# Kernel optimization log

Hardware: AMD Instinct MI355X
Metric: run time of the kernel (lower is better)

Reference implementation:

```python
import jax, jax.numpy as jnp
from jax import lax
import numpy as np

PADDING = 1
STRIDE = 1


def setup_inputs() -> dict:
    key = jax.random.key(0)
    k1, k2 = jax.random.split(key)
    x = jax.random.normal(k1, (256, 224, 224), dtype=jnp.float32)       # [C, H, W]
    kernel = jax.random.normal(k2, (256, 256, 3, 3), dtype=jnp.float32)  # [O, C, kh, kw]
    return {"x": x, "kernel": kernel}


def reference(x, kernel):
    # Direct conv2d with zero padding and stride, equivalent to the
    # nested-loop torch implementation (cross-correlation, no bias).
    out = lax.conv_general_dilated(
        x[None],                      # [1, C, H, W]
        kernel,                       # [O, C, kh, kw]
        window_strides=(STRIDE, STRIDE),
        padding=[(PADDING, PADDING), (PADDING, PADDING)],
        dimension_numbers=("NCHW", "OIHW", "NCHW"),
    )
    return out[0]                     # [O, Hout, Wout]
```

## Files before the change

kernel.cpp:

```cpp
#include <hip/hip_runtime.h>
#include <hip/hip_bf16.h>
#include <stdint.h>

#define C_IN  256
#define C_OUT 256
#define H_IN  224
#define W_IN  224
#define HP    226
#define WP    226
#define NPIX  (H_IN * W_IN)
#define BM    128
#define BN    128
#define BK    64

typedef __attribute__((ext_vector_type(8))) short short8;
typedef __attribute__((ext_vector_type(4))) float f32x4;

__device__ __forceinline__ unsigned short f2bf(float f) {
    __hip_bfloat16 b = __float2bfloat16(f);
    return *(unsigned short*)&b;
}

__device__ __forceinline__ void gl_lds16(const unsigned short* g, unsigned short* l) {
    __builtin_amdgcn_global_load_lds(
        (const __attribute__((address_space(1))) unsigned int*)g,
        (__attribute__((address_space(3))) unsigned int*)l,
        16, 0, 0);
}


__global__ void zero_border(unsigned short* __restrict__ xp) {
    int i = blockIdx.x * 256 + threadIdx.x;
    uint4 z = make_uint4(0u, 0u, 0u, 0u);
    if (i < 7232) {
        ((uint4*)xp)[i] = z;
    } else if (i < 14464) {
        ((uint4*)(xp + (size_t)225 * WP * C_IN))[i - 7232] = z;
    } else if (i < 21632) {
        int j = i - 14464; int h = 1 + (j >> 5); int c4 = j & 31;
        ((uint4*)(xp + ((size_t)h * WP) * C_IN))[c4] = z;
    } else if (i < 28800) {
        int j = i - 21632; int h = 1 + (j >> 5); int c4 = j & 31;
        ((uint4*)(xp + ((size_t)h * WP + 225) * C_IN))[c4] = z;
    }
}

__global__ void prep_x(const float* __restrict__ x, unsigned short* __restrict__ xp) {
    int b  = blockIdx.x;
    int ct = b & 3, wt = (b >> 2) & 3, h = b >> 4;
    int c0 = ct * 64, w0 = wt * 64;
    int t  = threadIdx.x;
    __shared__ float tile[64][65];

    int w   = t & 63;
    int cl0 = t >> 6;
    #pragma unroll
    for (int i = 0; i < 16; ++i) {
        int cl = i * 4 + cl0;
        float v = 0.f;
        if (w0 + w < W_IN)
            v = x[(size_t)(c0 + cl) * NPIX + (size_t)h * W_IN + w0 + w];
        tile[cl][w] = v;
    }
    __syncthreads();

    int wc = t >> 2;
    int cc = (t & 3) * 16;
    if (w0 + wc < W_IN) {
        uint32_t pk[8];
        #pragma unroll
        for (int j = 0; j < 8; ++j) {
            unsigned short lo = f2bf(tile[cc + 2 * j][wc]);
            unsigned short hi = f2bf(tile[cc + 2 * j + 1][wc]);
            pk[j] = (uint32_t)lo | ((uint32_t)hi << 16);
        }
        size_t base = ((size_t)(h + 1) * WP + (w0 + wc + 1)) * C_IN + c0 + cc;
        uint4* dst = (uint4*)(xp + base);
        dst[0] = make_uint4(pk[0], pk[1], pk[2], pk[3]);
        dst[1] = make_uint4(pk[4], pk[5], pk[6], pk[7]);
    }
}

__global__ void prep_w(const float* __restrict__ wk, unsigned short* __restrict__ wb) {
    int idx = blockIdx.x * 256 + threadIdx.x;
    int c = idx & 255, o = (idx >> 8) & 255, p = idx >> 16;
    wb[((size_t)p * 256 + o) * 256 + c] = f2bf(wk[((size_t)o * 256 + c) * 9 + p]);
}


__launch_bounds__(256, 2)
__global__ void conv_gemm(const unsigned short* __restrict__ xp,
                          const unsigned short* __restrict__ wb,
                          float* __restrict__ out) {
    int wgid = (blockIdx.x & 7) * 98 + (blockIdx.x >> 3);
    int mt = wgid & 1;
    int nt = wgid >> 1;
    int m0 = mt * BM;
    int n0 = nt * BN;
    int t  = threadIdx.x;
    int l  = t & 63, wv = t >> 6;

    __shared__ __align__(16) unsigned short lds[2 * 16384];

    int q8 = ((l & 7) ^ (l >> 3)) * 8;
    int rA = l >> 3;
    int offA0, offA1, offA2, offA3, offB0, offB1, offB2, offB3;
    {
        int r0 = (wv * 4 + 0) * 8 + rA;
        int r1 = (wv * 4 + 1) * 8 + rA;
        int r2 = (wv * 4 + 2) * 8 + rA;
        int r3 = (wv * 4 + 3) * 8 + rA;
        offA0 = (m0 + r0) * C_IN + q8;
        offA1 = (m0 + r1) * C_IN + q8;
        offA2 = (m0 + r2) * C_IN + q8;
        offA3 = (m0 + r3) * C_IN + q8;
        int nc0 = n0 + r0, nc1 = n0 + r1, nc2 = n0 + r2, nc3 = n0 + r3;
        int h0 = nc0 / W_IN, h1 = nc1 / W_IN, h2 = nc2 / W_IN, h3 = nc3 / W_IN;
        offB0 = (h0 * WP + (nc0 - h0 * W_IN)) * C_IN + q8;
        offB1 = (h1 * WP + (nc1 - h1 * W_IN)) * C_IN + q8;
        offB2 = (h2 * WP + (nc2 - h2 * W_IN)) * C_IN + q8;
        offB3 = (h3 * WP + (nc3 - h3 * W_IN)) * C_IN + q8;
    }

    int la = l & 15;
    int lk = l >> 4;
    int mo = (wv >> 1) * 64;
    int no = (wv & 1) * 64;
    int xq0 = ((0 * 4 + lk) ^ (la & 7)) * 8;
    int xq1 = ((1 * 4 + lk) ^ (la & 7)) * 8;

    f32x4 acc[4][4];
    #pragma unroll
    for (int i = 0; i < 4; ++i)
        #pragma unroll
        for (int j = 0; j < 4; ++j)
            acc[i][j] = f32x4{0.f, 0.f, 0.f, 0.f};

#define STAGE(BD, S) do {                                                    \
    int s_ = (S);                                                            \
    int p_ = s_ >> 2, cs_ = (s_ & 3) << 6;                                   \
    int kh_ = (p_ * 11) >> 5; int kw_ = p_ - 3 * kh_;                        \
    const unsigned short* aS_ = wb + p_ * 65536 + cs_;                       \
    const unsigned short* bS_ = xp + (kh_ * WP + kw_) * C_IN + cs_;          \
    gl_lds16(aS_ + offA0, &lds[(BD) * 16384 + (wv * 4 + 0) * 512]);          \
    gl_lds16(aS_ + offA1, &lds[(BD) * 16384 + (wv * 4 + 1) * 512]);          \
    gl_lds16(aS_ + offA2, &lds[(BD) * 16384 + (wv * 4 + 2) * 512]);          \
    gl_lds16(aS_ + offA3, &lds[(BD) * 16384 + (wv * 4 + 3) * 512]);          \
    gl_lds16(bS_ + offB0, &lds[(BD) * 16384 + 8192 + (wv * 4 + 0) * 512]);   \
    gl_lds16(bS_ + offB1, &lds[(BD) * 16384 + 8192 + (wv * 4 + 1) * 512]);   \
    gl_lds16(bS_ + offB2, &lds[(BD) * 16384 + 8192 + (wv * 4 + 2) * 512]);   \
    gl_lds16(bS_ + offB3, &lds[(BD) * 16384 + 8192 + (wv * 4 + 3) * 512]);   \
} while (0)

#define COMPUTE(BC) do {                                                     \
    short8 af_[4][2], bf_[4][2];                                             \
    _Pragma("unroll")                                                        \
    for (int i_ = 0; i_ < 4; ++i_) {                                         \
        af_[i_][0] = *(const short8*)&lds[(BC) * 16384 + (mo + i_ * 16 + la) * BK + xq0]; \
        af_[i_][1] = *(const short8*)&lds[(BC) * 16384 + (mo + i_ * 16 + la) * BK + xq1]; \
    }                                                                        \
    _Pragma("unroll")                                                        \
    for (int i_ = 0; i_ < 4; ++i_) {                                         \
        bf_[i_][0] = *(const short8*)&lds[(BC) * 16384 + 8192 + (no + i_ * 16 + la) * BK + xq0]; \
        bf_[i_][1] = *(const short8*)&lds[(BC) * 16384 + 8192 + (no + i_ * 16 + la) * BK + xq1]; \
    }                                                                        \
    __builtin_amdgcn_s_setprio(1);                                           \
    _Pragma("unroll")                                                        \
    for (int i_ = 0; i_ < 4; ++i_)                                           \
        _Pragma("unroll")                                                    \
        for (int j_ = 0; j_ < 4; ++j_)                                       \
            acc[i_][j_] = __builtin_amdgcn_mfma_f32_16x16x32_bf16(           \
                af_[i_][0], bf_[j_][0], acc[i_][j_], 0, 0, 0);               \
    _Pragma("unroll")                                                        \
    for (int i_ = 0; i_ < 4; ++i_)                                           \
        _Pragma("unroll")                                                    \
        for (int j_ = 0; j_ < 4; ++j_)                                       \
            acc[i_][j_] = __builtin_amdgcn_mfma_f32_16x16x32_bf16(           \
                af_[i_][1], bf_[j_][1], acc[i_][j_], 0, 0, 0);               \
    __builtin_amdgcn_s_setprio(0);                                           \
} while (0)

#define GUARD_IN(VMSTR) do {                                                 \
    asm volatile("s_waitcnt " VMSTR ::: "memory");                           \
    __builtin_amdgcn_sched_barrier(0);                                       \
    __builtin_amdgcn_s_barrier();                                            \
    __builtin_amdgcn_sched_barrier(0);                                       \
} while (0)

#define GUARD_OUT() do {                                                     \
    asm volatile("s_waitcnt lgkmcnt(0)" ::: "memory");                       \
    __builtin_amdgcn_sched_barrier(0);                                       \
    __builtin_amdgcn_s_barrier();                                            \
    __builtin_amdgcn_sched_barrier(0);                                       \
} while (0)

#define BODY(BC, S) do {                                                     \
    STAGE((BC) ^ 1, (S) + 1);                                                \
    GUARD_IN("vmcnt(8)");                                                    \
    COMPUTE(BC);                                                             \
    GUARD_OUT();                                                             \
} while (0)

    STAGE(0, 0);
    #pragma unroll 1
    for (int k = 0; k < 17; ++k) {
        BODY(0, 2 * k);
        BODY(1, 2 * k + 1);
    }
    BODY(0, 34);
    GUARD_IN("vmcnt(0)");
    COMPUTE(1);

#undef BODY
#undef GUARD_OUT
#undef GUARD_IN
#undef COMPUTE
#undef STAGE

    int ro = lk * 4;
    #pragma unroll
    for (int i = 0; i < 4; ++i) {
        #pragma unroll
        for (int j = 0; j < 4; ++j) {
            int oo = m0 + mo + i * 16 + ro;
            int nn = n0 + no + j * 16 + la;
            #pragma unroll
            for (int r = 0; r < 4; ++r)
                out[(size_t)(oo + r) * NPIX + nn] = acc[i][j][r];
        }
    }
}

__global__ void conv_naive(const float* __restrict__ x, const float* __restrict__ wk,
                           float* __restrict__ out) {
    int idx = blockIdx.x * 256 + threadIdx.x;
    int n = idx % NPIX;
    int o = idx / NPIX;
    int h = n / W_IN, w = n - (n / W_IN) * W_IN;
    float s = 0.f;
    for (int c = 0; c < C_IN; ++c) {
        const float* xc = x + (size_t)c * NPIX;
        const float* wc = wk + ((size_t)o * C_IN + c) * 9;
        #pragma unroll
        for (int kh = 0; kh < 3; ++kh) {
            int hh = h + kh - 1;
            if (hh < 0 || hh >= H_IN) continue;
            #pragma unroll
            for (int kw = 0; kw < 3; ++kw) {
                int ww = w + kw - 1;
                if (ww < 0 || ww >= W_IN) continue;
                s += xc[hh * W_IN + ww] * wc[kh * 3 + kw];
            }
        }
    }
    out[idx] = s;
}

extern "C" void kernel_launch(void* const* d_in, const int* in_sizes, int n_in,
                              void* d_out, int out_size, void* d_ws, size_t ws_size,
                              hipStream_t stream) {
    const float* x  = (const float*)d_in[0];
    const float* wk = (const float*)d_in[1];
    float* out = (float*)d_out;

    const size_t xp_elems = (size_t)HP * WP * C_IN;
    const size_t wb_elems = (size_t)9 * 256 * 256;
    const size_t need = (xp_elems + wb_elems) * 2;

    if (ws_size < need) {
        conv_naive<<<(C_OUT * NPIX) / 256, 256, 0, stream>>>(x, wk, out);
        return;
    }

    unsigned short* xp = (unsigned short*)d_ws;
    unsigned short* wb = xp + xp_elems;

    zero_border<<<113, 256, 0, stream>>>(xp);
    prep_x<<<224 * 16, 256, 0, stream>>>(x, xp);
    prep_w<<<2304, 256, 0, stream>>>(wk, wb);
    conv_gemm<<<392 * 2, 256, 0, stream>>>(xp, wb, out);
}
```

Measured before the change: 88.47 us.

## Merge weight prep with border zeroing and split LDS reads around MFMA halves

Weight conversion and border zeroing now run as one launch instead of two, removing one kernel launch. The GEMM main loop is reorganised: each iteration waits for the previous prefetch, loads half of the K fragments from LDS, issues the next stage's global-to-LDS prefetch, runs 16 MFMAs, then loads the second half and runs the rest. This interleaves LDS reads with MFMA work and trims register pressure. The trade-off is vmcnt(0) at the top of every iteration, so the prefetch now has only one compute phase to hide behind instead of overlapping freely.

```diff
diff --git a/kernel.cpp b/kernel.cpp
--- a/kernel.cpp
+++ b/kernel.cpp
@@ -29,8 +29,16 @@
 }
 
 
-__global__ void zero_border(unsigned short* __restrict__ xp) {
-    int i = blockIdx.x * 256 + threadIdx.x;
+__global__ void prep_misc(const float* __restrict__ wk, unsigned short* __restrict__ wb,
+                          unsigned short* __restrict__ xp) {
+    int b = blockIdx.x;
+    if (b < 2304) {
+        int idx = b * 256 + threadIdx.x;
+        int c = idx & 255, o = (idx >> 8) & 255, p = idx >> 16;
+        wb[((size_t)p * 256 + o) * 256 + c] = f2bf(wk[((size_t)o * 256 + c) * 9 + p]);
+        return;
+    }
+    int i = (b - 2304) * 256 + threadIdx.x;
     uint4 z = make_uint4(0u, 0u, 0u, 0u);
     if (i < 7232) {
         ((uint4*)xp)[i] = z;
@@ -79,12 +87,6 @@
         dst[0] = make_uint4(pk[0], pk[1], pk[2], pk[3]);
         dst[1] = make_uint4(pk[4], pk[5], pk[6], pk[7]);
     }
-}
-
-__global__ void prep_w(const float* __restrict__ wk, unsigned short* __restrict__ wb) {
-    int idx = blockIdx.x * 256 + threadIdx.x;
-    int c = idx & 255, o = (idx >> 8) & 255, p = idx >> 16;
-    wb[((size_t)p * 256 + o) * 256 + c] = f2bf(wk[((size_t)o * 256 + c) * 9 + p]);
 }
 
 
@@ -152,69 +154,60 @@
     gl_lds16(bS_ + offB3, &lds[(BD) * 16384 + 8192 + (wv * 4 + 3) * 512]);   \
 } while (0)
 
-#define COMPUTE(BC) do {                                                     \
-    short8 af_[4][2], bf_[4][2];                                             \
-    _Pragma("unroll")                                                        \
-    for (int i_ = 0; i_ < 4; ++i_) {                                         \
-        af_[i_][0] = *(const short8*)&lds[(BC) * 16384 + (mo + i_ * 16 + la) * BK + xq0]; \
-        af_[i_][1] = *(const short8*)&lds[(BC) * 16384 + (mo + i_ * 16 + la) * BK + xq1]; \
-    }                                                                        \
-    _Pragma("unroll")                                                        \
-    for (int i_ = 0; i_ < 4; ++i_) {                                         \
-        bf_[i_][0] = *(const short8*)&lds[(BC) * 16384 + 8192 + (no + i_ * 16 + la) * BK + xq0]; \
-        bf_[i_][1] = *(const short8*)&lds[(BC) * 16384 + 8192 + (no + i_ * 16 + la) * BK + xq1]; \
-    }                                                                        \
+#define MFMA16(AF, BF) do {                                                  \
     __builtin_amdgcn_s_setprio(1);                                           \
     _Pragma("unroll")                                                        \
     for (int i_ = 0; i_ < 4; ++i_)                                           \
         _Pragma("unroll")                                                    \
         for (int j_ = 0; j_ < 4; ++j_)                                       \
             acc[i_][j_] = __builtin_amdgcn_mfma_f32_16x16x32_bf16(           \
-                af_[i_][0], bf_[j_][0], acc[i_][j_], 0, 0, 0);               \
+                AF[i_], BF[j_], acc[i_][j_], 0, 0, 0);                       \
+    __builtin_amdgcn_s_setprio(0);                                           \
+} while (0)
+
+#define LGKM0() do {                                                         \
+    asm volatile("s_waitcnt lgkmcnt(0)" ::: "memory");                       \
+    __builtin_amdgcn_sched_barrier(0);                                       \
+} while (0)
+
+#define BODY(BC, S, DO_STAGE) do {                                           \
+    asm volatile("s_waitcnt vmcnt(0)" ::: "memory");                         \
+    __builtin_amdgcn_sched_barrier(0);                                       \
+    __builtin_amdgcn_s_barrier();                                            \
+    __builtin_amdgcn_sched_barrier(0);                                       \
+    short8 a0_[4], b0_[4], a1_[4], b1_[4];                                   \
     _Pragma("unroll")                                                        \
-    for (int i_ = 0; i_ < 4; ++i_)                                           \
-        _Pragma("unroll")                                                    \
-        for (int j_ = 0; j_ < 4; ++j_)                                       \
-            acc[i_][j_] = __builtin_amdgcn_mfma_f32_16x16x32_bf16(           \
-                af_[i_][1], bf_[j_][1], acc[i_][j_], 0, 0, 0);               \
-    __builtin_amdgcn_s_setprio(0);                                           \
-} while (0)
-
-#define GUARD_IN(VMSTR) do {                                                 \
-    asm volatile("s_waitcnt " VMSTR ::: "memory");                           \
+    for (int i_ = 0; i_ < 4; ++i_) {                                         \
+        a0_[i_] = *(const short8*)&lds[(BC) * 16384 + (mo + i_ * 16 + la) * BK + xq0]; \
+        b0_[i_] = *(const short8*)&lds[(BC) * 16384 + 8192 + (no + i_ * 16 + la) * BK + xq0]; \
+    }                                                                        \
+    if (DO_STAGE) STAGE((BC) ^ 1, (S) + 1);                                  \
+    LGKM0();                                                                 \
+    MFMA16(a0_, b0_);                                                        \
+    _Pragma("unroll")                                                        \
+    for (int i_ = 0; i_ < 4; ++i_) {                                         \
+        a1_[i_] = *(const short8*)&lds[(BC) * 16384 + (mo + i_ * 16 + la) * BK + xq1]; \
+        b1_[i_] = *(const short8*)&lds[(BC) * 16384 + 8192 + (no + i_ * 16 + la) * BK + xq1]; \
+    }                                                                        \
+    LGKM0();                                                                 \
+    MFMA16(a1_, b1_);                                                        \
     __builtin_amdgcn_sched_barrier(0);                                       \
     __builtin_amdgcn_s_barrier();                                            \
     __builtin_amdgcn_sched_barrier(0);                                       \
-} while (0)
-
-#define GUARD_OUT() do {                                                     \
-    asm volatile("s_waitcnt lgkmcnt(0)" ::: "memory");                       \
-    __builtin_amdgcn_sched_barrier(0);                                       \
-    __builtin_amdgcn_s_barrier();                                            \
-    __builtin_amdgcn_sched_barrier(0);                                       \
-} while (0)
-
-#define BODY(BC, S) do {                                                     \
-    STAGE((BC) ^ 1, (S) + 1);                                                \
-    GUARD_IN("vmcnt(8)");                                                    \
-    COMPUTE(BC);                                                             \
-    GUARD_OUT();                                                             \
 } while (0)
 
     STAGE(0, 0);
     #pragma unroll 1
     for (int k = 0; k < 17; ++k) {
-        BODY(0, 2 * k);
-        BODY(1, 2 * k + 1);
-    }
-    BODY(0, 34);
-    GUARD_IN("vmcnt(0)");
-    COMPUTE(1);
+        BODY(0, 2 * k, 1);
+        BODY(1, 2 * k + 1, 1);
+    }
+    BODY(0, 34, 1);
+    BODY(1, 35, 0);
 
 #undef BODY
-#undef GUARD_OUT
-#undef GUARD_IN
-#undef COMPUTE
+#undef LGKM0
+#undef MFMA16
 #undef STAGE
 
     int ro = lk * 4;
@@ -275,8 +268,7 @@
     unsigned short* xp = (unsigned short*)d_ws;
     unsigned short* wb = xp + xp_elems;
 
-    zero_border<<<113, 256, 0, stream>>>(xp);
+    prep_misc<<<2304 + 113, 256, 0, stream>>>(wk, wb, xp);
     prep_x<<<224 * 16, 256, 0, stream>>>(x, xp);
-    prep_w<<<2304, 256, 0, stream>>>(wk, wb);
     conv_gemm<<<392 * 2, 256, 0, stream>>>(xp, wb, out);
 }
```

Measured after the change: 95.15 us. 1.08x slower.
